# Performance work log

Measured on AMD Instinct MI355X. Metric: run time of the kernel, lower is better.

## Reference

```python
import jax, jax.numpy as jnp
import numpy as np

E, D, DFF = 8, 1024, 4096

def setup_inputs() -> dict:
    key = jax.random.key(0)
    ks = jax.random.split(key, 10)
    s = 0.02
    return {
        "x":  jax.random.normal(ks[0], (4, 2048, D), dtype=jnp.float32),
        "Wr": jax.random.normal(ks[1], (D, E), dtype=jnp.float32) * s,
        "br": jnp.zeros((E,), dtype=jnp.float32),
        "W1": jax.random.normal(ks[2], (E, D, DFF), dtype=jnp.float32) * s,
        "b1": jnp.zeros((E, DFF), dtype=jnp.float32),
        "W2": jax.random.normal(ks[3], (E, D, DFF), dtype=jnp.float32) * s,
        "b2": jnp.zeros((E, DFF), dtype=jnp.float32),
        "W3": jax.random.normal(ks[4], (E, DFF, D), dtype=jnp.float32) * s,
        "b3": jnp.zeros((E, D), dtype=jnp.float32),
    }

def reference(x, Wr, br, W1, b1, W2, b2, W3, b3):
    b, s, d = x.shape
    xt = x.reshape(b * s, d)                       # [T, D]
    logits = xt @ Wr + br                          # [T, E]
    pr, idx = jax.lax.top_k(logits, 2)             # [T, 2]
    w = jax.nn.softmax(pr, axis=-1)                # softmax over the 2 selected experts
    # combine weight per (token, expert): sum of routing weights where expert selected
    onehot = jax.nn.one_hot(idx, W1.shape[0], dtype=x.dtype)  # [T, 2, E]
    cw = jnp.einsum('tk,tke->te', w, onehot)       # [T, E]
    y = jnp.zeros_like(xt)
    for e in range(W1.shape[0]):                   # small fixed expert loop
        h = jax.nn.silu(xt @ W1[e] + b1[e]) * (xt @ W2[e] + b2[e])  # SwiGLU [T, DFF]
        y = y + (h @ W3[e] + b3[e]) * cw[:, e:e + 1]
    return y.reshape(b, s, d)
```

## Files before the change

### kernel.cpp

```cpp
#include <hip/hip_runtime.h>

#define T_TOK 8192
#define DIM   1024
#define DFF_  4096
#define NE    8
#define MAXT  144

typedef float  f32x4 __attribute__((ext_vector_type(4)));
typedef __bf16 b16x8 __attribute__((ext_vector_type(8)));

__device__ __forceinline__ unsigned short f2bf(float f) {
  union { float f; unsigned int u; } v; v.f = f;
  unsigned int r = v.u + 0x7fffu + ((v.u >> 16) & 1u);
  return (unsigned short)(r >> 16);
}

__device__ __forceinline__ void gload_lds16(const void* g, void* l) {
  __builtin_amdgcn_global_load_lds((const __attribute__((address_space(1))) void*)g,
                                   (__attribute__((address_space(3))) void*)l,
                                   16, 0, 0);
}

#define DRAIN_VMCNT() asm volatile("s_waitcnt vmcnt(0)" ::: "memory")

__global__ __launch_bounds__(256) void transpose_cvt(const float* __restrict__ src,
                                                     unsigned short* __restrict__ dst,
                                                     int R, int C) {
  __shared__ float tile[64][65];
  size_t mat = (size_t)blockIdx.z * R * C;
  int c0 = blockIdx.x * 64, r0 = blockIdx.y * 64;
  int lc = threadIdx.x & 63, q = threadIdx.x >> 6;
  const float* s = src + mat + (size_t)r0 * C + c0;
#pragma unroll
  for (int i = 0; i < 16; i++) {
    int r = q + i * 4;
    tile[r][lc] = s[(size_t)r * C + lc];
  }
  __syncthreads();
  unsigned short* d = dst + mat + (size_t)c0 * R + r0;
  int lc2 = (threadIdx.x & 31) * 2, cq = threadIdx.x >> 5;
#pragma unroll
  for (int i = 0; i < 8; i++) {
    int cc = cq + i * 8;
    unsigned lo = f2bf(tile[lc2][cc]);
    unsigned hi = f2bf(tile[lc2 + 1][cc]);
    *(unsigned*)(&d[(size_t)cc * R + lc2]) = lo | (hi << 16);
  }
}

__global__ __launch_bounds__(256) void router_k(const float* __restrict__ x,
                                                const float* __restrict__ Wr,
                                                const float* __restrict__ br,
                                                unsigned short* __restrict__ Xbf,
                                                int* __restrict__ top2e,
                                                float* __restrict__ top2w,
                                                int* __restrict__ counts) {
  __shared__ int lcnt[NE];
  if (threadIdx.x < NE) lcnt[threadIdx.x] = 0;
  __syncthreads();
  int wid = threadIdx.x >> 6, lane = threadIdx.x & 63;
  int t = blockIdx.x * 4 + wid;
  const float* xr = x + (size_t)t * DIM;
  unsigned short* xb = Xbf + (size_t)t * DIM;
  float s[NE];
#pragma unroll
  for (int e = 0; e < NE; e++) s[e] = 0.f;
  for (int i = 0; i < DIM / 64; i++) {
    int dd = i * 64 + lane;
    float xv = xr[dd];
    xb[dd] = f2bf(xv);
    const float* w = Wr + (size_t)dd * NE;
#pragma unroll
    for (int e = 0; e < NE; e++) s[e] += xv * w[e];
  }
#pragma unroll
  for (int m = 32; m >= 1; m >>= 1) {
#pragma unroll
    for (int e = 0; e < NE; e++) s[e] += __shfl_xor(s[e], m, 64);
  }
  if (lane == 0) {
#pragma unroll
    for (int e = 0; e < NE; e++) s[e] += br[e];
    int e0 = 0;
#pragma unroll
    for (int e = 1; e < NE; e++) if (s[e] > s[e0]) e0 = e;
    int e1 = (e0 == 0) ? 1 : 0;
#pragma unroll
    for (int e = 0; e < NE; e++) if (e != e0 && s[e] > s[e1]) e1 = e;
    float w0 = 1.f / (1.f + expf(s[e1] - s[e0]));
    top2e[2 * t] = e0; top2e[2 * t + 1] = e1;
    top2w[2 * t] = w0; top2w[2 * t + 1] = 1.f - w0;
    atomicAdd(&lcnt[e0], 1);
    atomicAdd(&lcnt[e1], 1);
  }
  __syncthreads();
  if (threadIdx.x < NE) atomicAdd(&counts[threadIdx.x], lcnt[threadIdx.x]);
}

__global__ void scan_build(int* __restrict__ ctrl) {
  if (threadIdx.x != 0 || blockIdx.x != 0) return;
  int* counts = ctrl;
  int* offsets = ctrl + 8;
  int* cursors = ctrl + 16;
  int* ntile = ctrl + 24;
  int* tileE = ctrl + 32;
  int* tileM = ctrl + 32 + MAXT;
  int o = 0;
  for (int e = 0; e < NE; e++) { offsets[e] = o; cursors[e] = o; o += counts[e]; }
  int nt = 0;
  for (int e = 0; e < NE; e++)
    for (int m0 = 0; m0 < counts[e]; m0 += 128) { tileE[nt] = e; tileM[nt] = m0; nt++; }
  ntile[0] = nt;
}

__global__ __launch_bounds__(256) void scatter_k(const int* __restrict__ top2e,
                                                 const float* __restrict__ top2w,
                                                 int* __restrict__ cursors,
                                                 int* __restrict__ list_tok,
                                                 float* __restrict__ list_w) {
  __shared__ int lcnt[NE];
  __shared__ int lbase[NE];
  int tid = threadIdx.x;
  if (tid < NE) lcnt[tid] = 0;
  __syncthreads();
  int t = blockIdx.x * 256 + tid;
  int e0 = top2e[2 * t], e1 = top2e[2 * t + 1];
  int r0 = atomicAdd(&lcnt[e0], 1);
  int r1 = atomicAdd(&lcnt[e1], 1);
  __syncthreads();
  if (tid < NE) lbase[tid] = atomicAdd(&cursors[tid], lcnt[tid]);
  __syncthreads();
  int p0 = lbase[e0] + r0, p1 = lbase[e1] + r1;
  list_tok[p0] = t; list_w[p0] = top2w[2 * t];
  list_tok[p1] = t; list_w[p1] = top2w[2 * t + 1];
}

__global__ __launch_bounds__(512) void gemm1_k(const unsigned short* __restrict__ Xbf,
                                               const unsigned short* __restrict__ W1T,
                                               const unsigned short* __restrict__ W2T,
                                               const float* __restrict__ b1,
                                               const float* __restrict__ b2,
                                               unsigned short* __restrict__ H,
                                               const int* __restrict__ list_tok,
                                               const int* __restrict__ ctrl) {
  const int* counts = ctrl; const int* offsets = ctrl + 8;
  const int* ntile = ctrl + 24;
  const int* tileE = ctrl + 32; const int* tileM = ctrl + 32 + MAXT;
  int bt = blockIdx.y;
  if (bt >= ntile[0]) return;
  int e = tileE[bt], m0 = tileM[bt];
  int Me = counts[e], off = offsets[e];
  int n0 = blockIdx.x * 128;

  __shared__ unsigned short lds[2][3 * 128 * 32];

  int tid = threadIdx.x, lane = tid & 63, wid = tid >> 6;
  int wr = wid >> 2, wc = wid & 3;

  const unsigned short* gsrc[3];
  unsigned ldsoff[3];
  {
    int lr = lane >> 2;
    int sc = ((lane & 3) ^ ((lane >> 3) & 3)) * 8;
#pragma unroll
    for (int j = 0; j < 3; j++) {
      int c = wid * 3 + j;
      ldsoff[j] = c * 512;
      if (c < 8) {
        int r = c * 16 + lr;
        int tok = (m0 + r < Me) ? list_tok[off + m0 + r] : list_tok[off];
        gsrc[j] = Xbf + (size_t)tok * DIM + sc;
      } else if (c < 16) {
        int n = n0 + (c - 8) * 16 + lr;
        gsrc[j] = W1T + ((size_t)e * DFF_ + n) * DIM + sc;
      } else {
        int n = n0 + (c - 16) * 16 + lr;
        gsrc[j] = W2T + ((size_t)e * DFF_ + n) * DIM + sc;
      }
    }
  }

  unsigned aoff[4], boff[2];
  {
    int colg = lane >> 4;
#pragma unroll
    for (int fi = 0; fi < 4; fi++) {
      int row = wr * 64 + fi * 16 + (lane & 15);
      aoff[fi] = row * 32 + ((colg ^ ((row >> 1) & 3)) * 8);
    }
#pragma unroll
    for (int fj = 0; fj < 2; fj++) {
      int row = wc * 32 + fj * 16 + (lane & 15);
      boff[fj] = row * 32 + ((colg ^ ((row >> 1) & 3)) * 8);
    }
  }

  f32x4 acc1[4][2], acc2[4][2];
#pragma unroll
  for (int i = 0; i < 4; i++)
#pragma unroll
    for (int j = 0; j < 2; j++) {
      acc1[i][j] = f32x4{0.f, 0.f, 0.f, 0.f};
      acc2[i][j] = f32x4{0.f, 0.f, 0.f, 0.f};
    }

  auto compute = [&](const unsigned short* base) {
    const unsigned short* sA  = base;
    const unsigned short* sB1 = base + 4096;
    const unsigned short* sB2 = base + 8192;
    b16x8 aF[4], bF1[2], bF2[2];
#pragma unroll
    for (int fi = 0; fi < 4; fi++) aF[fi] = *(const b16x8*)(sA + aoff[fi]);
#pragma unroll
    for (int fj = 0; fj < 2; fj++) {
      bF1[fj] = *(const b16x8*)(sB1 + boff[fj]);
      bF2[fj] = *(const b16x8*)(sB2 + boff[fj]);
    }
#pragma unroll
    for (int fi = 0; fi < 4; fi++)
#pragma unroll
      for (int fj = 0; fj < 2; fj++) {
        acc1[fi][fj] = __builtin_amdgcn_mfma_f32_16x16x32_bf16(aF[fi], bF1[fj], acc1[fi][fj], 0, 0, 0);
        acc2[fi][fj] = __builtin_amdgcn_mfma_f32_16x16x32_bf16(aF[fi], bF2[fj], acc2[fi][fj], 0, 0, 0);
      }
  };

#pragma unroll
  for (int j = 0; j < 3; j++) gload_lds16(gsrc[j], (void*)(&lds[0][ldsoff[j]]));
  DRAIN_VMCNT();
  __syncthreads();

  int cur = 0;
  const int NK = DIM / 32;
  for (int kt = 0; kt < NK; kt++) {
    if (kt + 1 < NK) {
#pragma unroll
      for (int j = 0; j < 3; j++)
        gload_lds16(gsrc[j] + (kt + 1) * 32, (void*)(&lds[cur ^ 1][ldsoff[j]]));
    }
    compute(&lds[cur][0]);
    DRAIN_VMCNT();
    __syncthreads();
    cur ^= 1;
  }

#pragma unroll
  for (int fi = 0; fi < 4; fi++)
#pragma unroll
    for (int fj = 0; fj < 2; fj++) {
      int col = n0 + wc * 32 + fj * 16 + (lane & 15);
      float bb1 = b1[e * DFF_ + col], bb2 = b2[e * DFF_ + col];
      int rbase = wr * 64 + fi * 16 + (lane >> 4) * 4;
#pragma unroll
      for (int r = 0; r < 4; r++) {
        int rr = rbase + r;
        if (m0 + rr < Me) {
          float c1 = acc1[fi][fj][r] + bb1;
          float c2 = acc2[fi][fj][r] + bb2;
          float h = c1 * c2 / (1.f + __expf(-c1));
          H[(size_t)(off + m0 + rr) * DFF_ + col] = f2bf(h);
        }
      }
    }
}

__global__ __launch_bounds__(512) void gemm2_k(const unsigned short* __restrict__ H,
                                               const unsigned short* __restrict__ W3T,
                                               const float* __restrict__ b3,
                                               const int* __restrict__ list_tok,
                                               const float* __restrict__ list_w,
                                               float* __restrict__ y,
                                               const int* __restrict__ ctrl) {
  const int* counts = ctrl; const int* offsets = ctrl + 8;
  const int* ntile = ctrl + 24;
  const int* tileE = ctrl + 32; const int* tileM = ctrl + 32 + MAXT;
  int bt = blockIdx.y;
  if (bt >= ntile[0]) return;
  int e = tileE[bt], m0 = tileM[bt];
  int Me = counts[e], off = offsets[e];
  int n0 = blockIdx.x * 128;

  __shared__ unsigned short lds[2][2 * 128 * 64];

  int tid = threadIdx.x, lane = tid & 63, wid = tid >> 6;
  int wr = wid >> 2, wc = wid & 3;

  const unsigned short* gsrc[4];
  unsigned ldsoff[4];
  {
    int lr = lane >> 3;
    int sc = ((lane & 7) ^ (lane >> 3)) * 8;
#pragma unroll
    for (int j = 0; j < 4; j++) {
      int c = wid * 4 + j;
      ldsoff[j] = c * 512;
      if (c < 16) {
        int r = c * 8 + lr;
        int pos = (m0 + r < Me) ? (off + m0 + r) : off;
        gsrc[j] = H + (size_t)pos * DFF_ + sc;
      } else {
        int n = n0 + (c - 16) * 8 + lr;
        gsrc[j] = W3T + ((size_t)e * DIM + n) * DFF_ + sc;
      }
    }
  }

  unsigned aoff[2][4], boff[2][2];
  {
    int colg = lane >> 4;
#pragma unroll
    for (int kk = 0; kk < 2; kk++) {
#pragma unroll
      for (int fi = 0; fi < 4; fi++) {
        int row = wr * 64 + fi * 16 + (lane & 15);
        aoff[kk][fi] = row * 64 + (((kk * 4 + colg) ^ (row & 7)) * 8);
      }
#pragma unroll
      for (int fj = 0; fj < 2; fj++) {
        int row = wc * 32 + fj * 16 + (lane & 15);
        boff[kk][fj] = row * 64 + (((kk * 4 + colg) ^ (row & 7)) * 8);
      }
    }
  }

  f32x4 acc[4][2];
#pragma unroll
  for (int i = 0; i < 4; i++)
#pragma unroll
    for (int j = 0; j < 2; j++) acc[i][j] = f32x4{0.f, 0.f, 0.f, 0.f};

  auto compute = [&](const unsigned short* base) {
    const unsigned short* sA = base;
    const unsigned short* sB = base + 128 * 64;
#pragma unroll
    for (int kk = 0; kk < 2; kk++) {
      b16x8 aF[4], bF[2];
#pragma unroll
      for (int fi = 0; fi < 4; fi++) aF[fi] = *(const b16x8*)(sA + aoff[kk][fi]);
#pragma unroll
      for (int fj = 0; fj < 2; fj++) bF[fj] = *(const b16x8*)(sB + boff[kk][fj]);
#pragma unroll
      for (int fi = 0; fi < 4; fi++)
#pragma unroll
        for (int fj = 0; fj < 2; fj++)
          acc[fi][fj] = __builtin_amdgcn_mfma_f32_16x16x32_bf16(aF[fi], bF[fj], acc[fi][fj], 0, 0, 0);
    }
  };

#pragma unroll
  for (int j = 0; j < 4; j++) gload_lds16(gsrc[j], (void*)(&lds[0][ldsoff[j]]));
  DRAIN_VMCNT();
  __syncthreads();

  int cur = 0;
  const int NK = DFF_ / 64;
  for (int kt = 0; kt < NK; kt++) {
    if (kt + 1 < NK) {
#pragma unroll
      for (int j = 0; j < 4; j++)
        gload_lds16(gsrc[j] + (kt + 1) * 64, (void*)(&lds[cur ^ 1][ldsoff[j]]));
    }
    compute(&lds[cur][0]);
    DRAIN_VMCNT();
    __syncthreads();
    cur ^= 1;
  }

#pragma unroll
  for (int fi = 0; fi < 4; fi++)
#pragma unroll
    for (int fj = 0; fj < 2; fj++) {
      int col = n0 + wc * 32 + fj * 16 + (lane & 15);
      float bb3 = b3[e * DIM + col];
      int rbase = wr * 64 + fi * 16 + (lane >> 4) * 4;
#pragma unroll
      for (int r = 0; r < 4; r++) {
        int rr = rbase + r;
        if (m0 + rr < Me) {
          int pos = off + m0 + rr;
          float v = list_w[pos] * (acc[fi][fj][r] + bb3);
          atomicAdd(&y[(size_t)list_tok[pos] * DIM + col], v);
        }
      }
    }
}

extern "C" void kernel_launch(void* const* d_in, const int* in_sizes, int n_in,
                              void* d_out, int out_size, void* d_ws, size_t ws_size,
                              hipStream_t stream) {
  (void)in_sizes; (void)n_in; (void)ws_size;
  const float* x  = (const float*)d_in[0];
  const float* Wr = (const float*)d_in[1];
  const float* br = (const float*)d_in[2];
  const float* W1 = (const float*)d_in[3];
  const float* b1 = (const float*)d_in[4];
  const float* W2 = (const float*)d_in[5];
  const float* b2 = (const float*)d_in[6];
  const float* W3 = (const float*)d_in[7];
  const float* b3 = (const float*)d_in[8];
  float* y = (float*)d_out;
  char* ws = (char*)d_ws;

  const size_t matB = (size_t)NE * DFF_ * DIM * 2;
  size_t oW1T = 0;
  size_t oW2T = oW1T + matB;
  size_t oXbf = oW2T + matB;
  size_t oH   = oXbf + (size_t)T_TOK * DIM * 2;
  size_t oT2e = oH + (size_t)2 * T_TOK * DFF_ * 2;
  size_t oT2w = oT2e + (size_t)2 * T_TOK * 4;
  size_t oLtk = oT2w + (size_t)2 * T_TOK * 4;
  size_t oLw  = oLtk + (size_t)2 * T_TOK * 4;
  size_t oCtl = oLw + (size_t)2 * T_TOK * 4;

  unsigned short* W1T = (unsigned short*)(ws + oW1T);
  unsigned short* W2T = (unsigned short*)(ws + oW2T);
  unsigned short* W3T = (unsigned short*)(ws + oW1T);
  unsigned short* Xbf = (unsigned short*)(ws + oXbf);
  unsigned short* Hb  = (unsigned short*)(ws + oH);
  int*   top2e = (int*)(ws + oT2e);
  float* top2w = (float*)(ws + oT2w);
  int*   ltok  = (int*)(ws + oLtk);
  float* lw    = (float*)(ws + oLw);
  int*   ctrl  = (int*)(ws + oCtl);

  hipMemsetAsync(y, 0, (size_t)out_size * 4, stream);
  hipMemsetAsync(ctrl, 0, (32 + 2 * MAXT) * 4, stream);

  transpose_cvt<<<dim3(DFF_ / 64, DIM / 64, NE), 256, 0, stream>>>(W1, W1T, DIM, DFF_);
  transpose_cvt<<<dim3(DFF_ / 64, DIM / 64, NE), 256, 0, stream>>>(W2, W2T, DIM, DFF_);
  router_k<<<dim3(T_TOK / 4), 256, 0, stream>>>(x, Wr, br, Xbf, top2e, top2w, ctrl);
  scan_build<<<dim3(1), 64, 0, stream>>>(ctrl);
  scatter_k<<<dim3(T_TOK / 256), 256, 0, stream>>>(top2e, top2w, ctrl + 16, ltok, lw);
  gemm1_k<<<dim3(DFF_ / 128, MAXT - 8), 512, 0, stream>>>(Xbf, W1T, W2T, b1, b2, Hb, ltok, ctrl);
  transpose_cvt<<<dim3(DIM / 64, DFF_ / 64, NE), 256, 0, stream>>>(W3, W3T, DFF_, DIM);
  gemm2_k<<<dim3(DIM / 128, MAXT - 8), 512, 0, stream>>>(Hb, W3T, b3, ltok, lw, y, ctrl);
}
```

Measured before the change: 771.1 us.

## Enlarge GEMM tiles to 256 rows, add 4-stage LDS pipeline, vectorize transpose

Both expert GEMMs now use 256-row token tiles with a 4x4 MFMA fragment block per wave. The old double-buffered loop that drained all loads every step becomes a 4-deep LDS ring with partial vmcnt waits, split barriers and s_setprio around the MFMA bursts. The weight transpose/convert kernel now uses float4 loads and 4-wide bf16 stores. The aim is more reuse of each loaded operand, latency hiding and fewer transpose memory transactions, at the cost of more registers and LDS, fewer blocks, and more padded rows in each expert's last tile.

```diff
diff --git a/kernel.cpp b/kernel.cpp
--- a/kernel.cpp
+++ b/kernel.cpp
@@ -8,6 +8,7 @@
 
 typedef float  f32x4 __attribute__((ext_vector_type(4)));
 typedef __bf16 b16x8 __attribute__((ext_vector_type(8)));
+typedef unsigned short u16x4 __attribute__((ext_vector_type(4)));
 
 __device__ __forceinline__ unsigned short f2bf(float f) {
   union { float f; unsigned int u; } v; v.f = f;
@@ -21,30 +22,37 @@
                                    16, 0, 0);
 }
 
-#define DRAIN_VMCNT() asm volatile("s_waitcnt vmcnt(0)" ::: "memory")
+#define WAITCNT(n) asm volatile("s_waitcnt vmcnt(" #n ")" ::: "memory")
+#define SBAR() do { asm volatile("" ::: "memory"); __builtin_amdgcn_s_barrier(); \
+                    asm volatile("" ::: "memory"); } while (0)
 
 __global__ __launch_bounds__(256) void transpose_cvt(const float* __restrict__ src,
                                                      unsigned short* __restrict__ dst,
                                                      int R, int C) {
-  __shared__ float tile[64][65];
+  __shared__ float tile[64][68];
   size_t mat = (size_t)blockIdx.z * R * C;
   int c0 = blockIdx.x * 64, r0 = blockIdx.y * 64;
-  int lc = threadIdx.x & 63, q = threadIdx.x >> 6;
+  int t = threadIdx.x;
+  int rcol = (t & 15) * 4, rrow = t >> 4;
   const float* s = src + mat + (size_t)r0 * C + c0;
 #pragma unroll
-  for (int i = 0; i < 16; i++) {
-    int r = q + i * 4;
-    tile[r][lc] = s[(size_t)r * C + lc];
+  for (int i = 0; i < 4; i++) {
+    int r = rrow + i * 16;
+    f32x4 v = *(const f32x4*)(s + (size_t)r * C + rcol);
+    *(f32x4*)(&tile[r][rcol]) = v;
   }
   __syncthreads();
   unsigned short* d = dst + mat + (size_t)c0 * R + r0;
-  int lc2 = (threadIdx.x & 31) * 2, cq = threadIdx.x >> 5;
-#pragma unroll
-  for (int i = 0; i < 8; i++) {
-    int cc = cq + i * 8;
-    unsigned lo = f2bf(tile[lc2][cc]);
-    unsigned hi = f2bf(tile[lc2 + 1][cc]);
-    *(unsigned*)(&d[(size_t)cc * R + lc2]) = lo | (hi << 16);
+  int wrow4 = (t & 15) * 4, wcol = t >> 4;
+#pragma unroll
+  for (int i = 0; i < 4; i++) {
+    int cc = wcol + i * 16;
+    u16x4 o;
+    o[0] = f2bf(tile[wrow4 + 0][cc]);
+    o[1] = f2bf(tile[wrow4 + 1][cc]);
+    o[2] = f2bf(tile[wrow4 + 2][cc]);
+    o[3] = f2bf(tile[wrow4 + 3][cc]);
+    *(u16x4*)(&d[(size_t)cc * R + wrow4]) = o;
   }
 }
 
@@ -109,7 +117,7 @@
   for (int e = 0; e < NE; e++) { offsets[e] = o; cursors[e] = o; o += counts[e]; }
   int nt = 0;
   for (int e = 0; e < NE; e++)
-    for (int m0 = 0; m0 < counts[e]; m0 += 128) { tileE[nt] = e; tileM[nt] = m0; nt++; }
+    for (int m0 = 0; m0 < counts[e]; m0 += 256) { tileE[nt] = e; tileM[nt] = m0; nt++; }
   ntile[0] = nt;
 }
 
@@ -152,116 +160,131 @@
   int Me = counts[e], off = offsets[e];
   int n0 = blockIdx.x * 128;
 
-  __shared__ unsigned short lds[2][3 * 128 * 32];
+  __shared__ unsigned short lds[4][16384];
 
   int tid = threadIdx.x, lane = tid & 63, wid = tid >> 6;
-  int wr = wid >> 2, wc = wid & 3;
-
-  const unsigned short* gsrc[3];
-  unsigned ldsoff[3];
+  int wr = wid >> 1, wc = wid & 1;
+
+  const unsigned short* gsrc[4];
+  unsigned ldsoff[4];
   {
     int lr = lane >> 2;
     int sc = ((lane & 3) ^ ((lane >> 3) & 3)) * 8;
 #pragma unroll
-    for (int j = 0; j < 3; j++) {
-      int c = wid * 3 + j;
+    for (int j = 0; j < 4; j++) {
+      int c = wid * 4 + j;
       ldsoff[j] = c * 512;
-      if (c < 8) {
+      if (c < 16) {
         int r = c * 16 + lr;
         int tok = (m0 + r < Me) ? list_tok[off + m0 + r] : list_tok[off];
         gsrc[j] = Xbf + (size_t)tok * DIM + sc;
-      } else if (c < 16) {
-        int n = n0 + (c - 8) * 16 + lr;
-        gsrc[j] = W1T + ((size_t)e * DFF_ + n) * DIM + sc;
       } else {
-        int n = n0 + (c - 16) * 16 + lr;
-        gsrc[j] = W2T + ((size_t)e * DFF_ + n) * DIM + sc;
+        int br = (c - 16) * 16 + lr;
+        if (br < 128) gsrc[j] = W1T + ((size_t)e * DFF_ + (n0 + br)) * DIM + sc;
+        else          gsrc[j] = W2T + ((size_t)e * DFF_ + (n0 + br - 128)) * DIM + sc;
       }
     }
   }
 
-  unsigned aoff[4], boff[2];
+  unsigned aoff[4], b1off[4];
   {
     int colg = lane >> 4;
 #pragma unroll
-    for (int fi = 0; fi < 4; fi++) {
-      int row = wr * 64 + fi * 16 + (lane & 15);
-      aoff[fi] = row * 32 + ((colg ^ ((row >> 1) & 3)) * 8);
-    }
-#pragma unroll
-    for (int fj = 0; fj < 2; fj++) {
-      int row = wc * 32 + fj * 16 + (lane & 15);
-      boff[fj] = row * 32 + ((colg ^ ((row >> 1) & 3)) * 8);
-    }
-  }
-
-  f32x4 acc1[4][2], acc2[4][2];
+    for (int m = 0; m < 4; m++) {
+      int row = wr * 64 + m * 16 + (lane & 15);
+      aoff[m] = row * 32 + ((colg ^ ((row >> 1) & 3)) * 8);
+    }
+#pragma unroll
+    for (int n = 0; n < 4; n++) {
+      int row = wc * 64 + n * 16 + (lane & 15);
+      b1off[n] = 8192 + row * 32 + ((colg ^ ((row >> 1) & 3)) * 8);
+    }
+  }
+
+  f32x4 acc1[4][4], acc2[4][4];
 #pragma unroll
   for (int i = 0; i < 4; i++)
 #pragma unroll
-    for (int j = 0; j < 2; j++) {
+    for (int j = 0; j < 4; j++) {
       acc1[i][j] = f32x4{0.f, 0.f, 0.f, 0.f};
       acc2[i][j] = f32x4{0.f, 0.f, 0.f, 0.f};
     }
 
-  auto compute = [&](const unsigned short* base) {
-    const unsigned short* sA  = base;
-    const unsigned short* sB1 = base + 4096;
-    const unsigned short* sB2 = base + 8192;
-    b16x8 aF[4], bF1[2], bF2[2];
-#pragma unroll
-    for (int fi = 0; fi < 4; fi++) aF[fi] = *(const b16x8*)(sA + aoff[fi]);
-#pragma unroll
-    for (int fj = 0; fj < 2; fj++) {
-      bF1[fj] = *(const b16x8*)(sB1 + boff[fj]);
-      bF2[fj] = *(const b16x8*)(sB2 + boff[fj]);
-    }
-#pragma unroll
-    for (int fi = 0; fi < 4; fi++)
-#pragma unroll
-      for (int fj = 0; fj < 2; fj++) {
-        acc1[fi][fj] = __builtin_amdgcn_mfma_f32_16x16x32_bf16(aF[fi], bF1[fj], acc1[fi][fj], 0, 0, 0);
-        acc2[fi][fj] = __builtin_amdgcn_mfma_f32_16x16x32_bf16(aF[fi], bF2[fj], acc2[fi][fj], 0, 0, 0);
-      }
+  b16x8 aF[4];
+
+  auto phase0 = [&](const unsigned short* base) {
+    b16x8 bF[4];
+#pragma unroll
+    for (int m = 0; m < 4; m++) aF[m] = *(const b16x8*)(base + aoff[m]);
+#pragma unroll
+    for (int n = 0; n < 4; n++) bF[n] = *(const b16x8*)(base + b1off[n]);
+    __builtin_amdgcn_s_setprio(1);
+#pragma unroll
+    for (int m = 0; m < 4; m++)
+#pragma unroll
+      for (int n = 0; n < 4; n++)
+        acc1[m][n] = __builtin_amdgcn_mfma_f32_16x16x32_bf16(aF[m], bF[n], acc1[m][n], 0, 0, 0);
+    __builtin_amdgcn_s_setprio(0);
   };
-
-#pragma unroll
-  for (int j = 0; j < 3; j++) gload_lds16(gsrc[j], (void*)(&lds[0][ldsoff[j]]));
-  DRAIN_VMCNT();
-  __syncthreads();
-
-  int cur = 0;
+  auto phase1 = [&](const unsigned short* base) {
+    b16x8 bF[4];
+#pragma unroll
+    for (int n = 0; n < 4; n++) bF[n] = *(const b16x8*)(base + b1off[n] + 128 * 32);
+    __builtin_amdgcn_s_setprio(1);
+#pragma unroll
+    for (int m = 0; m < 4; m++)
+#pragma unroll
+      for (int n = 0; n < 4; n++)
+        acc2[m][n] = __builtin_amdgcn_mfma_f32_16x16x32_bf16(aF[m], bF[n], acc2[m][n], 0, 0, 0);
+    __builtin_amdgcn_s_setprio(0);
+  };
+
   const int NK = DIM / 32;
-  for (int kt = 0; kt < NK; kt++) {
-    if (kt + 1 < NK) {
-#pragma unroll
-      for (int j = 0; j < 3; j++)
-        gload_lds16(gsrc[j] + (kt + 1) * 32, (void*)(&lds[cur ^ 1][ldsoff[j]]));
-    }
-    compute(&lds[cur][0]);
-    DRAIN_VMCNT();
-    __syncthreads();
-    cur ^= 1;
-  }
-
-#pragma unroll
-  for (int fi = 0; fi < 4; fi++)
-#pragma unroll
-    for (int fj = 0; fj < 2; fj++) {
-      int col = n0 + wc * 32 + fj * 16 + (lane & 15);
-      float bb1 = b1[e * DFF_ + col], bb2 = b2[e * DFF_ + col];
-      int rbase = wr * 64 + fi * 16 + (lane >> 4) * 4;
+#pragma unroll
+  for (int tpre = 0; tpre < 3; tpre++)
+#pragma unroll
+    for (int j = 0; j < 4; j++)
+      gload_lds16(gsrc[j] + tpre * 32, (void*)(&lds[tpre][ldsoff[j]]));
+
+  for (int kt = 0; kt < NK - 3; kt++) {
+    const unsigned short* sb = &lds[kt & 3][0];
+    unsigned short* pb = &lds[(kt + 3) & 3][0];
+    gload_lds16(gsrc[0] + (kt + 3) * 32, (void*)(pb + ldsoff[0]));
+    gload_lds16(gsrc[1] + (kt + 3) * 32, (void*)(pb + ldsoff[1]));
+    WAITCNT(10);
+    SBAR();
+    phase0(sb);
+    gload_lds16(gsrc[2] + (kt + 3) * 32, (void*)(pb + ldsoff[2]));
+    gload_lds16(gsrc[3] + (kt + 3) * 32, (void*)(pb + ldsoff[3]));
+    phase1(sb);
+    SBAR();
+  }
+  { const unsigned short* sb = &lds[(NK - 3) & 3][0];
+    WAITCNT(8); SBAR(); phase0(sb); phase1(sb); }
+  { const unsigned short* sb = &lds[(NK - 2) & 3][0];
+    WAITCNT(4); SBAR(); phase0(sb); phase1(sb); }
+  { const unsigned short* sb = &lds[(NK - 1) & 3][0];
+    WAITCNT(0); SBAR(); phase0(sb); phase1(sb); }
+
+#pragma unroll
+  for (int n = 0; n < 4; n++) {
+    int col = n0 + wc * 64 + n * 16 + (lane & 15);
+    float bb1 = b1[e * DFF_ + col], bb2 = b2[e * DFF_ + col];
+#pragma unroll
+    for (int m = 0; m < 4; m++) {
+      int rbase = wr * 64 + m * 16 + (lane >> 4) * 4;
 #pragma unroll
       for (int r = 0; r < 4; r++) {
         int rr = rbase + r;
         if (m0 + rr < Me) {
-          float c1 = acc1[fi][fj][r] + bb1;
-          float c2 = acc2[fi][fj][r] + bb2;
+          float c1 = acc1[m][n][r] + bb1;
+          float c2 = acc2[m][n][r] + bb2;
           float h = c1 * c2 / (1.f + __expf(-c1));
           H[(size_t)(off + m0 + rr) * DFF_ + col] = f2bf(h);
         }
       }
     }
+  }
 }
 
 __global__ __launch_bounds__(512) void gemm2_k(const unsigned short* __restrict__ H,
@@ -280,109 +303,107 @@
   int Me = counts[e], off = offsets[e];
   int n0 = blockIdx.x * 128;
 
-  __shared__ unsigned short lds[2][2 * 128 * 64];
+  __shared__ unsigned short lds[4][12288];
 
   int tid = threadIdx.x, lane = tid & 63, wid = tid >> 6;
-  int wr = wid >> 2, wc = wid & 3;
-
-  const unsigned short* gsrc[4];
-  unsigned ldsoff[4];
+  int wr = wid >> 1, wc = wid & 1;
+
+  const unsigned short* gsrc[3];
+  unsigned ldsoff[3];
   {
-    int lr = lane >> 3;
-    int sc = ((lane & 7) ^ (lane >> 3)) * 8;
-#pragma unroll
-    for (int j = 0; j < 4; j++) {
-      int c = wid * 4 + j;
+    int lr = lane >> 2;
+    int sc = ((lane & 3) ^ ((lane >> 3) & 3)) * 8;
+#pragma unroll
+    for (int j = 0; j < 3; j++) {
+      int c = wid * 3 + j;
       ldsoff[j] = c * 512;
       if (c < 16) {
-        int r = c * 8 + lr;
+        int r = c * 16 + lr;
         int pos = (m0 + r < Me) ? (off + m0 + r) : off;
         gsrc[j] = H + (size_t)pos * DFF_ + sc;
       } else {
-        int n = n0 + (c - 16) * 8 + lr;
-        gsrc[j] = W3T + ((size_t)e * DIM + n) * DFF_ + sc;
+        int br = (c - 16) * 16 + lr;
+        gsrc[j] = W3T + ((size_t)e * DIM + (n0 + br)) * DFF_ + sc;
       }
     }
   }
 
-  unsigned aoff[2][4], boff[2][2];
+  unsigned aoff[4], boff[4];
   {
     int colg = lane >> 4;
 #pragma unroll
-    for (int kk = 0; kk < 2; kk++) {
-#pragma unroll
-      for (int fi = 0; fi < 4; fi++) {
-        int row = wr * 64 + fi * 16 + (lane & 15);
-        aoff[kk][fi] = row * 64 + (((kk * 4 + colg) ^ (row & 7)) * 8);
-      }
-#pragma unroll
-      for (int fj = 0; fj < 2; fj++) {
-        int row = wc * 32 + fj * 16 + (lane & 15);
-        boff[kk][fj] = row * 64 + (((kk * 4 + colg) ^ (row & 7)) * 8);
-      }
-    }
-  }
-
-  f32x4 acc[4][2];
+    for (int m = 0; m < 4; m++) {
+      int row = wr * 64 + m * 16 + (lane & 15);
+      aoff[m] = row * 32 + ((colg ^ ((row >> 1) & 3)) * 8);
+    }
+#pragma unroll
+    for (int n = 0; n < 4; n++) {
+      int row = wc * 64 + n * 16 + (lane & 15);
+      boff[n] = 8192 + row * 32 + ((colg ^ ((row >> 1) & 3)) * 8);
+    }
+  }
+
+  f32x4 acc[4][4];
 #pragma unroll
   for (int i = 0; i < 4; i++)
 #pragma unroll
-    for (int j = 0; j < 2; j++) acc[i][j] = f32x4{0.f, 0.f, 0.f, 0.f};
+    for (int j = 0; j < 4; j++) acc[i][j] = f32x4{0.f, 0.f, 0.f, 0.f};
 
   auto compute = [&](const unsigned short* base) {
-    const unsigned short* sA = base;
-    const unsigned short* sB = base + 128 * 64;
-#pragma unroll
-    for (int kk = 0; kk < 2; kk++) {
-      b16x8 aF[4], bF[2];
-#pragma unroll
-      for (int fi = 0; fi < 4; fi++) aF[fi] = *(const b16x8*)(sA + aoff[kk][fi]);
-#pragma unroll
-      for (int fj = 0; fj < 2; fj++) bF[fj] = *(const b16x8*)(sB + boff[kk][fj]);
-#pragma unroll
-      for (int fi = 0; fi < 4; fi++)
-#pragma unroll
-        for (int fj = 0; fj < 2; fj++)
-          acc[fi][fj] = __builtin_amdgcn_mfma_f32_16x16x32_bf16(aF[fi], bF[fj], acc[fi][fj], 0, 0, 0);
-    }
+    b16x8 aF[4], bF[4];
+#pragma unroll
+    for (int m = 0; m < 4; m++) aF[m] = *(const b16x8*)(base + aoff[m]);
+#pragma unroll
+    for (int n = 0; n < 4; n++) bF[n] = *(const b16x8*)(base + boff[n]);
+    __builtin_amdgcn_s_setprio(1);
+#pragma unroll
+    for (int m = 0; m < 4; m++)
+#pragma unroll
+      for (int n = 0; n < 4; n++)
+        acc[m][n] = __builtin_amdgcn_mfma_f32_16x16x32_bf16(aF[m], bF[n], acc[m][n], 0, 0, 0);
+    __builtin_amdgcn_s_setprio(0);
   };
 
-#pragma unroll
-  for (int j = 0; j < 4; j++) gload_lds16(gsrc[j], (void*)(&lds[0][ldsoff[j]]));
-  DRAIN_VMCNT();
-  __syncthreads();
-
-  int cur = 0;
-  const int NK = DFF_ / 64;
-  for (int kt = 0; kt < NK; kt++) {
-    if (kt + 1 < NK) {
-#pragma unroll
-      for (int j = 0; j < 4; j++)
-        gload_lds16(gsrc[j] + (kt + 1) * 64, (void*)(&lds[cur ^ 1][ldsoff[j]]));
-    }
-    compute(&lds[cur][0]);
-    DRAIN_VMCNT();
-    __syncthreads();
-    cur ^= 1;
-  }
-
-#pragma unroll
-  for (int fi = 0; fi < 4; fi++)
-#pragma unroll
-    for (int fj = 0; fj < 2; fj++) {
-      int col = n0 + wc * 32 + fj * 16 + (lane & 15);
-      float bb3 = b3[e * DIM + col];
-      int rbase = wr * 64 + fi * 16 + (lane >> 4) * 4;
+  const int NK = DFF_ / 32;
+#pragma unroll
+  for (int tpre = 0; tpre < 3; tpre++)
+#pragma unroll
+    for (int j = 0; j < 3; j++)
+      gload_lds16(gsrc[j] + tpre * 32, (void*)(&lds[tpre][ldsoff[j]]));
+
+  for (int kt = 0; kt < NK - 3; kt++) {
+    const unsigned short* sb = &lds[kt & 3][0];
+    unsigned short* pb = &lds[(kt + 3) & 3][0];
+    gload_lds16(gsrc[0] + (kt + 3) * 32, (void*)(pb + ldsoff[0]));
+    gload_lds16(gsrc[1] + (kt + 3) * 32, (void*)(pb + ldsoff[1]));
+    gload_lds16(gsrc[2] + (kt + 3) * 32, (void*)(pb + ldsoff[2]));
+    WAITCNT(9);
+    SBAR();
+    compute(sb);
+    SBAR();
+  }
+  { WAITCNT(6); SBAR(); compute(&lds[(NK - 3) & 3][0]); }
+  { WAITCNT(3); SBAR(); compute(&lds[(NK - 2) & 3][0]); }
+  { WAITCNT(0); SBAR(); compute(&lds[(NK - 1) & 3][0]); }
+
+#pragma unroll
+  for (int n = 0; n < 4; n++) {
+    int col = n0 + wc * 64 + n * 16 + (lane & 15);
+    float bb3 = b3[e * DIM + col];
+#pragma unroll
+    for (int m = 0; m < 4; m++) {
+      int rbase = wr * 64 + m * 16 + (lane >> 4) * 4;
 #pragma unroll
       for (int r = 0; r < 4; r++) {
         int rr = rbase + r;
         if (m0 + rr < Me) {
           int pos = off + m0 + rr;
-          float v = list_w[pos] * (acc[fi][fj][r] + bb3);
+          float v = list_w[pos] * (acc[m][n][r] + bb3);
           atomicAdd(&y[(size_t)list_tok[pos] * DIM + col], v);
         }
       }
     }
+  }
 }
 
 extern "C" void kernel_launch(void* const* d_in, const int* in_sizes, int n_in,
@@ -431,7 +452,7 @@
   router_k<<<dim3(T_TOK / 4), 256, 0, stream>>>(x, Wr, br, Xbf, top2e, top2w, ctrl);
   scan_build<<<dim3(1), 64, 0, stream>>>(ctrl);
   scatter_k<<<dim3(T_TOK / 256), 256, 0, stream>>>(top2e, top2w, ctrl + 16, ltok, lw);
-  gemm1_k<<<dim3(DFF_ / 128, MAXT - 8), 512, 0, stream>>>(Xbf, W1T, W2T, b1, b2, Hb, ltok, ctrl);
+  gemm1_k<<<dim3(DFF_ / 128, 71), 512, 0, stream>>>(Xbf, W1T, W2T, b1, b2, Hb, ltok, ctrl);
   transpose_cvt<<<dim3(DIM / 64, DFF_ / 64, NE), 256, 0, stream>>>(W3, W3T, DFF_, DIM);
-  gemm2_k<<<dim3(DIM / 128, MAXT - 8), 512, 0, stream>>>(Hb, W3T, b3, ltok, lw, y, ctrl);
-}
+  gemm2_k<<<dim3(DIM / 128, 71), 512, 0, stream>>>(Hb, W3T, b3, ltok, lw, y, ctrl);
+}
```

Result: slower. 862.6 us (+11.9%).
